# Kernel tuning notes

Measured on AMD Instinct MI355X. Metric: run time of the kernel, lower is better.

The kernel has to match this reference:

```python
import jax, jax.numpy as jnp
import numpy as np

B, N, D, H = 32, 8192, 128, 128


def setup_inputs() -> dict:
    key = jax.random.key(0)
    ks = jax.random.split(key, 9)
    s = lambda k, shp, fan: jax.random.normal(k, shp, jnp.float32) / np.sqrt(fan)
    return {
        "x": jax.random.normal(ks[0], (B, N, D), jnp.float32),
        "Wg1": s(ks[1], (D, H), D), "bg1": jnp.zeros((H,), jnp.float32),
        "Wg2": s(ks[2], (H, 1), H), "bg2": jnp.zeros((1,), jnp.float32),
        "Wn1": s(ks[3], (D, H), D), "bn1": jnp.zeros((H,), jnp.float32),
        "Wn2": s(ks[4], (H, H), H), "bn2": jnp.zeros((H,), jnp.float32),
    }


def reference(x, Wg1, bg1, Wg2, bg2, Wn1, bn1, Wn2, bn2):
    # gate_nn: Linear -> SiLU -> Linear(->1); scores per node
    gate = jnp.einsum("bnd,dh->bnh", x, Wg1) + bg1
    gate = jax.nn.silu(gate)
    gate = jnp.einsum("bnh,ho->bno", gate, Wg2) + bg2  # [B,N,1]
    # nn: Linear -> SiLU -> Linear; transformed node features
    h = jax.nn.silu(jnp.einsum("bnd,dh->bnh", x, Wn1) + bn1)
    h = jnp.einsum("bnh,hk->bnk", h, Wn2) + bn2  # [B,N,H]
    # segment softmax over nodes of each graph (segments == batch dim here)
    attn = jax.nn.softmax(gate, axis=1)  # [B,N,1]
    # weighted-sum pooling per graph
    return jnp.sum(attn * h, axis=1)  # [B,H]
```

## Files before the change

kernel.cpp:

```cpp
#include <hip/hip_runtime.h>

#define B_ 32
#define N_ 8192
#define D_ 128
#define H_ 128
#define R_ (B_ * N_)

typedef _Float16 f16;
typedef __attribute__((ext_vector_type(4))) _Float16 f16x4;
typedef __attribute__((ext_vector_type(8))) _Float16 f16x8;
typedef __attribute__((ext_vector_type(4))) float f32x4;

static constexpr size_t WPACK_OFF = 0;
static constexpr size_t VPART_OFF = 98304;
static constexpr size_t SPART_OFF = VPART_OFF + 512 * 128 * 4;

__device__ __forceinline__ float silu_f(float v) {
    return v / (1.0f + __expf(-v));
}

__device__ __forceinline__ f32x4 mfma16(f16x8 a, f16x8 b, f32x4 c) {
    return __builtin_amdgcn_mfma_f32_16x16x32_f16(a, b, c, 0, 0, 0);
}

__global__ void k0_prepack(const float* __restrict__ Wg1,
                           const float* __restrict__ Wn1,
                           const float* __restrict__ Wn2,
                           f16* __restrict__ wp) {
    int tid = blockIdx.x * 256 + threadIdx.x;
    int m    = tid >> 14;
    int r    = tid & 16383;
    int j    = r & 7;
    int lane = (r >> 3) & 63;
    int kc   = (r >> 9) & 3;
    int nt   = r >> 11;
    int k = kc * 32 + (lane >> 4) * 8 + j;
    int n = nt * 16 + (lane & 15);
    const float* W = (m == 0) ? Wg1 : (m == 1) ? Wn1 : Wn2;
    wp[tid] = (f16)W[k * 128 + n];
}

__global__ __launch_bounds__(512) void k1_fused(
        const float* __restrict__ x,
        const float* __restrict__ bg1, const float* __restrict__ wg2,
        const float* __restrict__ bg2, const float* __restrict__ bn1,
        const f16* __restrict__ wp,
        float* __restrict__ vpart, float* __restrict__ spart) {
    __shared__ f16 xlds[64 * 128];
    __shared__ f16 h1lds[64 * 128];
    __shared__ float gpart[8][64];
    __shared__ float ebuf[64];

    const int tid  = threadIdx.x;
    const int w    = tid >> 6;
    const int lane = tid & 63;
    const int q    = lane >> 4;
    const int c    = lane & 15;

    const f16x8* wpv = (const f16x8*)wp;
    f16x8 fg1[4], fn1[4], fn2[4];
#pragma unroll
    for (int kc = 0; kc < 4; ++kc) {
        int base = (w * 4 + kc) * 64 + lane;
        fg1[kc] = wpv[base];
        fn1[kc] = wpv[2048 + base];
        fn2[kc] = wpv[4096 + base];
    }
    float bg1q[4], wg2q[4], bn1q[4];
#pragma unroll
    for (int r = 0; r < 4; ++r) {
        int col = w * 16 + q * 4 + r;
        bg1q[r] = bg1[col];
        wg2q[r] = wg2[col];
        bn1q[r] = bn1[col];
    }
    const float bg2v = bg2[0];

    const int loh_e = (q * 16 + (c ^ q)) * 8;
    const int loh_o = (q * 16 + (c ^ (q | 4))) * 8;
    const int kc2 = w >> 1;
    const int q2  = (w & 1) * 2 + (q >> 1);
    const int v2  = ((kc2 & 1) << 2) | q2;
    const int h1w_base = kc2 * 512 + (q2 * 16 + (c ^ v2)) * 8 + (q & 1) * 4;

    float V[4] = {0.f, 0.f, 0.f, 0.f};
    float Sl = 0.f;

    const long rowbase = (long)blockIdx.x * 512;

    float4 pre[4];
    {
        const float4* xg = (const float4*)x + rowbase * 32;
#pragma unroll
        for (int s = 0; s < 4; ++s) pre[s] = xg[s * 512 + tid];
    }

    for (int t = 0; t < 8; ++t) {
        __syncthreads();

#pragma unroll
        for (int s = 0; s < 4; ++s) {
            int e   = s * 512 + tid;
            int row = e >> 5, c4 = e & 31;
            int mt = row >> 4, cc = row & 15;
            int kc = c4 >> 3, qq = (c4 >> 1) & 3, j = (c4 & 1) * 4;
            int sw = (c4 >> 1) & 7;
            int hidx = ((mt * 4 + kc) * 64 + qq * 16 + (cc ^ sw)) * 8 + j;
            float4 vv = pre[s];
            f16x4 hv = {(f16)vv.x, (f16)vv.y, (f16)vv.z, (f16)vv.w};
            *(f16x4*)&xlds[hidx] = hv;
        }
        __syncthreads();

        if (t < 7) {
            const float4* xg = (const float4*)x + (rowbase + (t + 1) * 64) * 32;
#pragma unroll
            for (int s = 0; s < 4; ++s) pre[s] = xg[s * 512 + tid];
        }

#pragma unroll
        for (int mt = 0; mt < 4; ++mt) {
            f16x8 a[4];
#pragma unroll
            for (int kc = 0; kc < 4; ++kc)
                a[kc] = *(const f16x8*)&xlds[(mt * 4 + kc) * 512 +
                                             ((kc & 1) ? loh_o : loh_e)];
            f32x4 ag = {0.f, 0.f, 0.f, 0.f};
            f32x4 an = {0.f, 0.f, 0.f, 0.f};
#pragma unroll
            for (int kc = 0; kc < 4; ++kc) {
                ag = mfma16(fg1[kc], a[kc], ag);
                an = mfma16(fn1[kc], a[kc], an);
            }
            f16x4 h4;
#pragma unroll
            for (int r = 0; r < 4; ++r) h4[r] = (f16)silu_f(an[r] + bn1q[r]);
            *(f16x4*)&h1lds[mt * 2048 + h1w_base] = h4;
            float p = 0.f;
#pragma unroll
            for (int r = 0; r < 4; ++r)
                p += silu_f(ag[r] + bg1q[r]) * wg2q[r];
            p += __shfl_xor(p, 16);
            p += __shfl_xor(p, 32);
            if (lane < 16) gpart[w][mt * 16 + lane] = p;
        }
        __syncthreads();

        if (tid < 64) {
            float g = bg2v;
#pragma unroll
            for (int w2 = 0; w2 < 8; ++w2) g += gpart[w2][tid];
            float e = __expf(g);
            ebuf[tid] = e;
            Sl += e;
        }
        __syncthreads();

#pragma unroll
        for (int mt = 0; mt < 4; ++mt) {
            f16x8 b[4];
#pragma unroll
            for (int kc = 0; kc < 4; ++kc)
                b[kc] = *(const f16x8*)&h1lds[(mt * 4 + kc) * 512 +
                                              ((kc & 1) ? loh_o : loh_e)];
            f32x4 acc = {0.f, 0.f, 0.f, 0.f};
#pragma unroll
            for (int kc = 0; kc < 4; ++kc)
                acc = mfma16(fn2[kc], b[kc], acc);
            float e = ebuf[mt * 16 + c];
#pragma unroll
            for (int r = 0; r < 4; ++r) V[r] += e * acc[r];
        }
    }

#pragma unroll
    for (int m = 1; m < 16; m <<= 1) {
#pragma unroll
        for (int r = 0; r < 4; ++r) V[r] += __shfl_xor(V[r], m);
    }
    if ((lane & 15) == 0) {
        float4 o = {V[0], V[1], V[2], V[3]};
        *(float4*)&vpart[(long)blockIdx.x * 128 + w * 16 + q * 4] = o;
    }
    if (w == 0) {
#pragma unroll
        for (int m = 1; m < 64; m <<= 1) Sl += __shfl_xor(Sl, m);
        if (lane == 0) spart[blockIdx.x] = Sl;
    }
}

__global__ void k2_combine(const float* __restrict__ vpart,
                           const float* __restrict__ spart,
                           const float* __restrict__ bn2,
                           float* __restrict__ out) {
    const int b = blockIdx.x;
    const int j = threadIdx.x;
    float v = 0.f, s = 0.f;
#pragma unroll
    for (int k = 0; k < 16; ++k) {
        v += vpart[(long)(b * 16 + k) * 128 + j];
        s += spart[b * 16 + k];
    }
    out[b * 128 + j] = v / s + bn2[j];
}

extern "C" void kernel_launch(void* const* d_in, const int* in_sizes, int n_in,
                              void* d_out, int out_size, void* d_ws, size_t ws_size,
                              hipStream_t stream) {
    const float* x   = (const float*)d_in[0];
    const float* Wg1 = (const float*)d_in[1];
    const float* bg1 = (const float*)d_in[2];
    const float* Wg2 = (const float*)d_in[3];
    const float* bg2 = (const float*)d_in[4];
    const float* Wn1 = (const float*)d_in[5];
    const float* bn1 = (const float*)d_in[6];
    const float* Wn2 = (const float*)d_in[7];
    const float* bn2 = (const float*)d_in[8];
    float* out = (float*)d_out;

    char* ws = (char*)d_ws;
    f16*   wp    = (f16*)(ws + WPACK_OFF);
    float* vpart = (float*)(ws + VPART_OFF);
    float* spart = (float*)(ws + SPART_OFF);

    k0_prepack<<<192, 256, 0, stream>>>(Wg1, Wn1, Wn2, wp);
    k1_fused<<<512, 512, 0, stream>>>(x, bg1, Wg2, bg2, bn1, wp, vpart, spart);
    k2_combine<<<32, 128, 0, stream>>>(vpart, spart, bn2, out);
}
```

Measured before the change: 223.4 us.

## Double block count, drop ebuf barrier, precompute LDS addresses, use rcp in SiLU

Launches 1024 blocks of 4 tiles each instead of 512 blocks of 8 tiles, which gives more blocks per graph for better CU fill on a 256-CU part. Every lane now computes the softmax exponentials from gpart directly, which removes the ebuf shared buffer and one barrier per tile; the top-of-loop barrier is also removed. The swizzled LDS store addresses are computed once outside the loop, and SiLU uses a hardware reciprocal in place of division. This duplicates exp work across waves, doubles the partial results that k2 must reduce, and relies on the remaining barriers to guard the xlds and h1lds reuse.

```diff
diff --git a/kernel.cpp b/kernel.cpp
--- a/kernel.cpp
+++ b/kernel.cpp
@@ -6,6 +6,9 @@
 #define H_ 128
 #define R_ (B_ * N_)
 
+#define NBLK 1024
+#define TILES 4
+
 typedef _Float16 f16;
 typedef __attribute__((ext_vector_type(4))) _Float16 f16x4;
 typedef __attribute__((ext_vector_type(8))) _Float16 f16x8;
@@ -13,10 +16,10 @@
 
 static constexpr size_t WPACK_OFF = 0;
 static constexpr size_t VPART_OFF = 98304;
-static constexpr size_t SPART_OFF = VPART_OFF + 512 * 128 * 4;
+static constexpr size_t SPART_OFF = VPART_OFF + (size_t)NBLK * 128 * 4;
 
 __device__ __forceinline__ float silu_f(float v) {
-    return v / (1.0f + __expf(-v));
+    return v * __builtin_amdgcn_rcpf(1.0f + __expf(-v));
 }
 
 __device__ __forceinline__ f32x4 mfma16(f16x8 a, f16x8 b, f32x4 c) {
@@ -49,7 +52,6 @@
     __shared__ f16 xlds[64 * 128];
     __shared__ f16 h1lds[64 * 128];
     __shared__ float gpart[8][64];
-    __shared__ float ebuf[64];
 
     const int tid  = threadIdx.x;
     const int w    = tid >> 6;
@@ -83,39 +85,40 @@
     const int v2  = ((kc2 & 1) << 2) | q2;
     const int h1w_base = kc2 * 512 + (q2 * 16 + (c ^ v2)) * 8 + (q & 1) * 4;
 
+    f16* sdst[4];
+#pragma unroll
+    for (int s = 0; s < 4; ++s) {
+        int e   = s * 512 + tid;
+        int row = e >> 5, c4 = e & 31;
+        int mt = row >> 4, cc = row & 15;
+        int kc = c4 >> 3, qq = (c4 >> 1) & 3, j = (c4 & 1) * 4;
+        int sw = (c4 >> 1) & 7;
+        sdst[s] = &xlds[((mt * 4 + kc) * 64 + qq * 16 + (cc ^ sw)) * 8 + j];
+    }
+
     float V[4] = {0.f, 0.f, 0.f, 0.f};
     float Sl = 0.f;
 
-    const long rowbase = (long)blockIdx.x * 512;
+    const long rowbase = (long)blockIdx.x * (TILES * 64);
+    const float4* xg = (const float4*)x + rowbase * 32;
 
     float4 pre[4];
-    {
-        const float4* xg = (const float4*)x + rowbase * 32;
-#pragma unroll
-        for (int s = 0; s < 4; ++s) pre[s] = xg[s * 512 + tid];
-    }
-
-    for (int t = 0; t < 8; ++t) {
-        __syncthreads();
-
+#pragma unroll
+    for (int s = 0; s < 4; ++s) pre[s] = xg[s * 512 + tid];
+
+    for (int t = 0; t < TILES; ++t) {
 #pragma unroll
         for (int s = 0; s < 4; ++s) {
-            int e   = s * 512 + tid;
-            int row = e >> 5, c4 = e & 31;
-            int mt = row >> 4, cc = row & 15;
-            int kc = c4 >> 3, qq = (c4 >> 1) & 3, j = (c4 & 1) * 4;
-            int sw = (c4 >> 1) & 7;
-            int hidx = ((mt * 4 + kc) * 64 + qq * 16 + (cc ^ sw)) * 8 + j;
             float4 vv = pre[s];
             f16x4 hv = {(f16)vv.x, (f16)vv.y, (f16)vv.z, (f16)vv.w};
-            *(f16x4*)&xlds[hidx] = hv;
+            *(f16x4*)sdst[s] = hv;
         }
         __syncthreads();
 
-        if (t < 7) {
-            const float4* xg = (const float4*)x + (rowbase + (t + 1) * 64) * 32;
-#pragma unroll
-            for (int s = 0; s < 4; ++s) pre[s] = xg[s * 512 + tid];
+        if (t < TILES - 1) {
+            const float4* xn = xg + (t + 1) * 2048;
+#pragma unroll
+            for (int s = 0; s < 4; ++s) pre[s] = xn[s * 512 + tid];
         }
 
 #pragma unroll
@@ -146,15 +149,18 @@
         }
         __syncthreads();
 
-        if (tid < 64) {
+        float e[4];
+#pragma unroll
+        for (int mt = 0; mt < 4; ++mt) {
             float g = bg2v;
 #pragma unroll
-            for (int w2 = 0; w2 < 8; ++w2) g += gpart[w2][tid];
-            float e = __expf(g);
-            ebuf[tid] = e;
-            Sl += e;
-        }
-        __syncthreads();
+            for (int w2 = 0; w2 < 8; ++w2) g += gpart[w2][mt * 16 + c];
+            e[mt] = __expf(g);
+        }
+        if (w == 0 && q == 0) {
+#pragma unroll
+            for (int mt = 0; mt < 4; ++mt) Sl += e[mt];
+        }
 
 #pragma unroll
         for (int mt = 0; mt < 4; ++mt) {
@@ -167,9 +173,8 @@
 #pragma unroll
             for (int kc = 0; kc < 4; ++kc)
                 acc = mfma16(fn2[kc], b[kc], acc);
-            float e = ebuf[mt * 16 + c];
-#pragma unroll
-            for (int r = 0; r < 4; ++r) V[r] += e * acc[r];
+#pragma unroll
+            for (int r = 0; r < 4; ++r) V[r] += e[mt] * acc[r];
         }
     }
 
@@ -184,7 +189,7 @@
     }
     if (w == 0) {
 #pragma unroll
-        for (int m = 1; m < 64; m <<= 1) Sl += __shfl_xor(Sl, m);
+        for (int m = 1; m < 16; m <<= 1) Sl += __shfl_xor(Sl, m);
         if (lane == 0) spart[blockIdx.x] = Sl;
     }
 }
@@ -195,11 +200,12 @@
                            float* __restrict__ out) {
     const int b = blockIdx.x;
     const int j = threadIdx.x;
+    const int P = NBLK / B_;
     float v = 0.f, s = 0.f;
 #pragma unroll
-    for (int k = 0; k < 16; ++k) {
-        v += vpart[(long)(b * 16 + k) * 128 + j];
-        s += spart[b * 16 + k];
+    for (int k = 0; k < P; ++k) {
+        v += vpart[(long)(b * P + k) * 128 + j];
+        s += spart[b * P + k];
     }
     out[b * 128 + j] = v / s + bn2[j];
 }
@@ -224,6 +230,6 @@
     float* spart = (float*)(ws + SPART_OFF);
 
     k0_prepack<<<192, 256, 0, stream>>>(Wg1, Wn1, Wn2, wp);
-    k1_fused<<<512, 512, 0, stream>>>(x, bg1, Wg2, bg2, bn1, wp, vpart, spart);
+    k1_fused<<<NBLK, 512, 0, stream>>>(x, bg1, Wg2, bg2, bn1, wp, vpart, spart);
     k2_combine<<<32, 128, 0, stream>>>(vpart, spart, bn2, out);
 }
```

New measurement: 221.2 us. Within noise of the previous version (-0.9%).
